# Kernel tuning notes

Hardware: AMD Instinct MI355X
Metric: run time of the kernel (lower is better)

The kernel has to match this reference:

```python
import jax, jax.numpy as jnp
import numpy as np

B, T, D, H, C = 256, 512, 64, 512, 1

def setup_inputs() -> dict:
    key = jax.random.key(0)
    ks = jax.random.split(key, 12)
    return {
        "x": jax.random.normal(ks[0], (B, T, D), jnp.float32),
        "w_ih_mu": jax.random.normal(ks[1], (D, 4 * H), jnp.float32) * 0.1,
        "w_ih_rho": jax.random.normal(ks[2], (D, 4 * H), jnp.float32) - 6.0,
        "eps_ih": jax.random.normal(ks[3], (D, 4 * H), jnp.float32),
        "w_hh_mu": jax.random.normal(ks[4], (H, 4 * H), jnp.float32) * 0.1,
        "w_hh_rho": jax.random.normal(ks[5], (H, 4 * H), jnp.float32) - 6.0,
        "eps_hh": jax.random.normal(ks[6], (H, 4 * H), jnp.float32),
        "b_mu": jax.random.normal(ks[7], (4 * H,), jnp.float32) * 0.1,
        "b_rho": jax.random.normal(ks[8], (4 * H,), jnp.float32) - 6.0,
        "eps_b": jax.random.normal(ks[9], (4 * H,), jnp.float32),
        "lin_w": jax.random.normal(ks[10], (C, H), jnp.float32) * 0.04,
        "lin_b": jax.random.normal(ks[11], (C,), jnp.float32) * 0.04,
    }

def _sample(mu, rho, eps):
    # blitz reparameterization: sigma = log1p(exp(rho))
    return mu + jnp.log1p(jnp.exp(rho)) * eps

def reference(x, w_ih_mu, w_ih_rho, eps_ih, w_hh_mu, w_hh_rho, eps_hh,
              b_mu, b_rho, eps_b, lin_w, lin_b):
    w_ih = _sample(w_ih_mu, w_ih_rho, eps_ih)
    w_hh = _sample(w_hh_mu, w_hh_rho, eps_hh)
    b = _sample(b_mu, b_rho, eps_b)

    # precompute input projections for all timesteps: [T, B, 4H]
    x_proj = jnp.einsum('btd,dg->tbg', x, w_ih) + b

    def step(carry, xp_t):
        h, c = carry
        gates = xp_t + h @ w_hh                      # [B, 4H]
        i, f, g, o = jnp.split(gates, 4, axis=-1)
        i = jax.nn.sigmoid(i)
        f = jax.nn.sigmoid(f)
        g = jnp.tanh(g)
        o = jax.nn.sigmoid(o)
        c = f * c + i * g
        h = o * jnp.tanh(c)
        return (h, c), None

    h0 = jnp.zeros((x.shape[0], w_hh.shape[0]), x.dtype)
    (h_last, _), _ = jax.lax.scan(step, (h0, h0), x_proj)
    # original takes outputs[:, -1, :] == last hidden state, then Linear
    return h_last @ lin_w.T + lin_b
```

## Files before the change

kernel.cpp:

```cpp
#include <hip/hip_runtime.h>

typedef unsigned short u16;
typedef unsigned long long u64;
typedef short v8s __attribute__((ext_vector_type(8)));
typedef float v4f __attribute__((ext_vector_type(4)));
typedef unsigned v2u __attribute__((ext_vector_type(2)));

#define Bb 256
#define Tt 512
#define Dd 64
#define Hh 512
#define G4 2048

#define NGROUP 16
#define NCHUNK 16
#define BT 16
#define HC 32
#define NCOL 128

#define WHH_S 520
#define WIH_S 72
#define SMEM_BYTES (NCOL*WHH_S*2 + NCOL*WIH_S*2)

#define MFMA(a,b,c) __builtin_amdgcn_mfma_f32_16x16x32_bf16((a),(b),(c),0,0,0)

__device__ __forceinline__ u16 f2bf(float f) {
  unsigned u = __float_as_uint(f);
  unsigned r = (u + 0x7fffu + ((u >> 16) & 1u)) >> 16;
  return (u16)r;
}
__device__ __forceinline__ float bf2f(u16 v) {
  return __uint_as_float(((unsigned)v) << 16);
}
__device__ __forceinline__ float sigm(float x) { return 1.0f / (1.0f + __expf(-x)); }
__device__ __forceinline__ float tanh_f(float x) {
  float a = fabsf(x);
  float e = __expf(-2.0f * a);
  float r = (1.0f - e) / (1.0f + e);
  return copysignf(r, x);
}
__device__ __forceinline__ float softplus_f(float x) { return log1pf(__expf(x)); }

__global__ void k_prep(const float* __restrict__ x, u16* __restrict__ x_bf,
                       unsigned* __restrict__ flags)
{
  if (blockIdx.x < 2) {
    int i = blockIdx.x * 256 + threadIdx.x;
    if (i < NGROUP * NCHUNK * 2) flags[i] = 0u;
  }
  const int N4 = Tt * Bb * Dd / 4;
  int stride = gridDim.x * blockDim.x;
  for (int i = blockIdx.x * blockDim.x + threadIdx.x; i < N4; i += stride) {
    int idx = i * 4;
    int t = idx >> 14;
    int rem = idx & 16383;
    int b = rem >> 6;
    int d = rem & 63;
    float4 v = *(const float4*)(x + (size_t)b * (Tt * Dd) + t * Dd + d);
    unsigned lo = (unsigned)f2bf(v.x) | ((unsigned)f2bf(v.y) << 16);
    unsigned hi = (unsigned)f2bf(v.z) | ((unsigned)f2bf(v.w) << 16);
    *(uint2*)(x_bf + idx) = make_uint2(lo, hi);
  }
}

__global__ __launch_bounds__(128, 1) void lstm_main(
    const float* __restrict__ whh_mu, const float* __restrict__ whh_rho, const float* __restrict__ whh_eps,
    const float* __restrict__ wih_mu, const float* __restrict__ wih_rho, const float* __restrict__ wih_eps,
    const float* __restrict__ b_mu,  const float* __restrict__ b_rho,  const float* __restrict__ b_eps,
    const u16* __restrict__ x_bf, u16* __restrict__ h_buf, unsigned* __restrict__ flags)
{
  extern __shared__ char smem[];
  u16* w_hh_lds = (u16*)smem;
  u16* w_ih_lds = w_hh_lds + NCOL * WHH_S;

  const int tid   = threadIdx.x;
  const int g     = blockIdx.x & 15;
  const int chunk = blockIdx.x >> 4;
  const int b0    = g * BT;
  const int j0    = chunk * HC;

  {
    const int lc = tid;
    const int gcol = (lc >> 5) * Hh + j0 + (lc & 31);
    #pragma unroll 4
    for (int k = 0; k < Hh; ++k) {
      int gi = k * G4 + gcol;
      float w = whh_mu[gi] + softplus_f(whh_rho[gi]) * whh_eps[gi];
      w_hh_lds[lc * WHH_S + k] = f2bf(w);
    }
    #pragma unroll 4
    for (int k = 0; k < Dd; ++k) {
      int gi = k * G4 + gcol;
      float w = wih_mu[gi] + softplus_f(wih_rho[gi]) * wih_eps[gi];
      w_ih_lds[lc * WIH_S + k] = f2bf(w);
    }
  }

  const int lane = tid & 63;
  const int wv   = tid >> 6;
  const int ln   = lane & 15;
  const int q    = lane >> 4;
  const int ko   = q * 8;

  const u16* WhP[4]; const u16* WxP[4];
  #pragma unroll
  for (int gt = 0; gt < 4; ++gt) {
    int rt = gt * 2 + wv;
    WhP[gt] = w_hh_lds + (rt * 16 + ln) * WHH_S + ko;
    WxP[gt] = w_ih_lds + (rt * 16 + ln) * WIH_S + ko;
  }

  const int bat = b0 + ln;

  float bs[4][4];
  #pragma unroll
  for (int gt = 0; gt < 4; ++gt)
    #pragma unroll
    for (int r = 0; r < 4; ++r) {
      int colg = gt * Hh + j0 + wv * 16 + q * 4 + r;
      bs[gt][r] = b_mu[colg] + softplus_f(b_rho[colg]) * b_eps[colg];
    }

  float cc[4] = {0.f, 0.f, 0.f, 0.f};
  unsigned* const fgrp2 = flags + g * (NCHUNK * 2);
  const unsigned* fp2 = fgrp2 + (lane & 31);
  __syncthreads();

  for (int t = 0; t < Tt; ++t) {
    v4f ac0 = {0.f,0.f,0.f,0.f}, ac1 = {0.f,0.f,0.f,0.f};
    v4f ac2 = {0.f,0.f,0.f,0.f}, ac3 = {0.f,0.f,0.f,0.f};

    {
      const u16* xb = x_bf + (size_t)t * (Bb * Dd) + bat * Dd + ko;
      #pragma unroll
      for (int ks = 0; ks < 2; ++ks) {
        v8s xf = *(const v8s*)(xb + ks * 32);
        ac0 = MFMA(*(const v8s*)(WxP[0] + ks * 32), xf, ac0);
        ac1 = MFMA(*(const v8s*)(WxP[1] + ks * 32), xf, ac1);
        ac2 = MFMA(*(const v8s*)(WxP[2] + ks * 32), xf, ac2);
        ac3 = MFMA(*(const v8s*)(WxP[3] + ks * 32), xf, ac3);
      }
    }

    if (t > 0) {
      const u16* hb = h_buf + (t & 1) * (Bb * Hh) + bat * Hh + ko;
      unsigned done = 0, todo = 0;
      v8s buf[16];
      for (;;) {
        unsigned pv = 0;
        bool needPoll = (done | todo) != 0xFFFFu;
        if (needPoll) {
          asm volatile("global_load_dword %0, %1, off sc0 sc1"
                       : "=v"(pv) : "v"(fp2));
        }
        #pragma unroll
        for (int c = 0; c < 16; ++c)
          if (todo & (1u << c)) {
            asm volatile("global_load_dwordx4 %0, %1, off offset:%c2 sc0 sc1"
                         : "=v"(buf[c]) : "v"(hb), "i"(c * 64));
          }
        asm volatile("s_waitcnt vmcnt(0)");
        if (needPoll) {
          asm volatile("" : "+v"(pv));
        }
        #pragma unroll
        for (int c = 0; c < 16; ++c)
          if (todo & (1u << c)) {
            asm volatile("" : "+v"(buf[c]));
            ac0 = MFMA(*(const v8s*)(WhP[0] + c * 32), buf[c], ac0);
            ac1 = MFMA(*(const v8s*)(WhP[1] + c * 32), buf[c], ac1);
            ac2 = MFMA(*(const v8s*)(WhP[2] + c * 32), buf[c], ac2);
            ac3 = MFMA(*(const v8s*)(WhP[3] + c * 32), buf[c], ac3);
          }
        done |= todo;
        if (done == 0xFFFFu) break;
        u64 bal = __ballot((int)(pv >= (unsigned)t));
        unsigned lo = (unsigned)bal;
        unsigned ready = lo & (lo >> 16) & 0xFFFFu;
        todo = ready & ~done;
      }
    }

    {
      u16 hv[4];
      #pragma unroll
      for (int r = 0; r < 4; ++r) {
        float ig = sigm  (ac0[r] + bs[0][r]);
        float fg = sigm  (ac1[r] + bs[1][r]);
        float gg = tanh_f(ac2[r] + bs[2][r]);
        float og = sigm  (ac3[r] + bs[3][r]);
        cc[r] = fg * cc[r] + ig * gg;
        hv[r] = f2bf(og * tanh_f(cc[r]));
      }
      v2u qv;
      qv[0] = (unsigned)hv[0] | ((unsigned)hv[1] << 16);
      qv[1] = (unsigned)hv[2] | ((unsigned)hv[3] << 16);
      u16* hp = h_buf + ((t + 1) & 1) * (Bb * Hh) + bat * Hh
              + j0 + wv * 16 + q * 4;
      asm volatile("global_store_dwordx2 %0, %1, off sc0 sc1"
                   :: "v"(hp), "v"(qv) : "memory");
    }

    asm volatile("s_waitcnt vmcnt(0)" ::: "memory");
    if (lane == 0) {
      unsigned tv = (unsigned)(t + 1);
      unsigned* fq = &fgrp2[wv * 16 + chunk];
      asm volatile("global_store_dword %0, %1, off sc0 sc1"
                   :: "v"(fq), "v"(tv) : "memory");
    }
  }
}

__global__ void k_out(const u16* __restrict__ h, const float* __restrict__ lw,
                      const float* __restrict__ lb, float* __restrict__ out)
{
  int b = blockIdx.x * 64 + threadIdx.x;
  if (b >= Bb) return;
  const u16* hr = h + b * Hh;
  float acc = 0.f;
  #pragma unroll 8
  for (int k = 0; k < Hh; ++k) acc += bf2f(hr[k]) * lw[k];
  out[b] = acc + lb[0];
}

extern "C" void kernel_launch(void* const* d_in, const int* in_sizes, int n_in,
                              void* d_out, int out_size, void* d_ws, size_t ws_size,
                              hipStream_t stream)
{
  (void)in_sizes; (void)n_in; (void)out_size; (void)ws_size;
  const float* x       = (const float*)d_in[0];
  const float* wih_mu  = (const float*)d_in[1];
  const float* wih_rho = (const float*)d_in[2];
  const float* wih_eps = (const float*)d_in[3];
  const float* whh_mu  = (const float*)d_in[4];
  const float* whh_rho = (const float*)d_in[5];
  const float* whh_eps = (const float*)d_in[6];
  const float* b_mu    = (const float*)d_in[7];
  const float* b_rho   = (const float*)d_in[8];
  const float* b_eps   = (const float*)d_in[9];
  const float* lin_w   = (const float*)d_in[10];
  const float* lin_b   = (const float*)d_in[11];
  float* out = (float*)d_out;

  u16* x_bf  = (u16*)d_ws;
  u16* h_buf = x_bf + (size_t)Tt * Bb * Dd;
  unsigned* flags = (unsigned*)(h_buf + 2 * Bb * Hh);

  k_prep<<<2048, 256, 0, stream>>>(x, x_bf, flags);

  hipFuncSetAttribute(reinterpret_cast<const void*>(lstm_main),
                      hipFuncAttributeMaxDynamicSharedMemorySize, SMEM_BYTES);
  lstm_main<<<NGROUP * NCHUNK, 128, SMEM_BYTES, stream>>>(
      whh_mu, whh_rho, whh_eps, wih_mu, wih_rho, wih_eps,
      b_mu, b_rho, b_eps, x_bf, h_buf, flags);

  k_out<<<(Bb + 63) / 64, 64, 0, stream>>>(h_buf, lin_w, lin_b, out);
}
```

Measured before the change: 2.473 ms.

## Split K dimension across waves with LDS reduction in recurrent LSTM step

Each wave now computes all 8 gate row tiles over half of the K dimension (256 of the hidden inputs and 32 of the input features) instead of 4 row tiles over the full K. The partial sums are exchanged through an LDS buffer with two block barriers per timestep. Each wave then waits on flags only for its own half of the h chunks, which shortens the dependency chain and lets the two waves consume producer data independently. In exchange each step adds LDS traffic, two __syncthreads calls, and twice as many accumulator registers.

```diff
diff --git a/kernel.cpp b/kernel.cpp
--- a/kernel.cpp
+++ b/kernel.cpp
@@ -20,7 +20,7 @@
 
 #define WHH_S 520
 #define WIH_S 72
-#define SMEM_BYTES (NCOL*WHH_S*2 + NCOL*WIH_S*2)
+#define SMEM_BYTES (NCOL*WHH_S*2 + NCOL*WIH_S*2 + 8192)
 
 #define MFMA(a,b,c) __builtin_amdgcn_mfma_f32_16x16x32_bf16((a),(b),(c),0,0,0)
 
@@ -70,8 +70,9 @@
     const u16* __restrict__ x_bf, u16* __restrict__ h_buf, unsigned* __restrict__ flags)
 {
   extern __shared__ char smem[];
-  u16* w_hh_lds = (u16*)smem;
-  u16* w_ih_lds = w_hh_lds + NCOL * WHH_S;
+  u16*   w_hh_lds = (u16*)smem;
+  u16*   w_ih_lds = w_hh_lds + NCOL * WHH_S;
+  float* pb       = (float*)(w_ih_lds + NCOL * WIH_S);
 
   const int tid   = threadIdx.x;
   const int g     = blockIdx.x & 15;
@@ -102,12 +103,11 @@
   const int q    = lane >> 4;
   const int ko   = q * 8;
 
-  const u16* WhP[4]; const u16* WxP[4];
+  const u16* WhB[8]; const u16* WxB[8];
   #pragma unroll
-  for (int gt = 0; gt < 4; ++gt) {
-    int rt = gt * 2 + wv;
-    WhP[gt] = w_hh_lds + (rt * 16 + ln) * WHH_S + ko;
-    WxP[gt] = w_ih_lds + (rt * 16 + ln) * WIH_S + ko;
+  for (int rt = 0; rt < 8; ++rt) {
+    WhB[rt] = w_hh_lds + (rt * 16 + ln) * WHH_S + wv * 256 + ko;
+    WxB[rt] = w_ih_lds + (rt * 16 + ln) * WIH_S + wv * 32 + ko;
   }
 
   const int bat = b0 + ln;
@@ -123,38 +123,35 @@
 
   float cc[4] = {0.f, 0.f, 0.f, 0.f};
   unsigned* const fgrp2 = flags + g * (NCHUNK * 2);
-  const unsigned* fp2 = fgrp2 + (lane & 31);
+  const unsigned* fp2 = fgrp2 + ((lane >> 3) & 1) * 16 + wv * 8 + (lane & 7);
   __syncthreads();
 
   for (int t = 0; t < Tt; ++t) {
-    v4f ac0 = {0.f,0.f,0.f,0.f}, ac1 = {0.f,0.f,0.f,0.f};
-    v4f ac2 = {0.f,0.f,0.f,0.f}, ac3 = {0.f,0.f,0.f,0.f};
+    v4f acc[8];
+    #pragma unroll
+    for (int rt = 0; rt < 8; ++rt) acc[rt] = (v4f){0.f,0.f,0.f,0.f};
 
     {
-      const u16* xb = x_bf + (size_t)t * (Bb * Dd) + bat * Dd + ko;
-      #pragma unroll
-      for (int ks = 0; ks < 2; ++ks) {
-        v8s xf = *(const v8s*)(xb + ks * 32);
-        ac0 = MFMA(*(const v8s*)(WxP[0] + ks * 32), xf, ac0);
-        ac1 = MFMA(*(const v8s*)(WxP[1] + ks * 32), xf, ac1);
-        ac2 = MFMA(*(const v8s*)(WxP[2] + ks * 32), xf, ac2);
-        ac3 = MFMA(*(const v8s*)(WxP[3] + ks * 32), xf, ac3);
-      }
+      const u16* xb = x_bf + (size_t)t * (Bb * Dd) + bat * Dd + wv * 32 + ko;
+      v8s xf = *(const v8s*)xb;
+      #pragma unroll
+      for (int rt = 0; rt < 8; ++rt)
+        acc[rt] = MFMA(*(const v8s*)WxB[rt], xf, acc[rt]);
     }
 
     if (t > 0) {
-      const u16* hb = h_buf + (t & 1) * (Bb * Hh) + bat * Hh + ko;
+      const u16* hb = h_buf + (t & 1) * (Bb * Hh) + bat * Hh + wv * 256 + ko;
       unsigned done = 0, todo = 0;
-      v8s buf[16];
+      v8s buf[8];
       for (;;) {
         unsigned pv = 0;
-        bool needPoll = (done | todo) != 0xFFFFu;
+        bool needPoll = (done | todo) != 0xFFu;
         if (needPoll) {
           asm volatile("global_load_dword %0, %1, off sc0 sc1"
                        : "=v"(pv) : "v"(fp2));
         }
         #pragma unroll
-        for (int c = 0; c < 16; ++c)
+        for (int c = 0; c < 8; ++c)
           if (todo & (1u << c)) {
             asm volatile("global_load_dwordx4 %0, %1, off offset:%c2 sc0 sc1"
                          : "=v"(buf[c]) : "v"(hb), "i"(c * 64));
@@ -164,31 +161,48 @@
           asm volatile("" : "+v"(pv));
         }
         #pragma unroll
-        for (int c = 0; c < 16; ++c)
+        for (int c = 0; c < 8; ++c)
           if (todo & (1u << c)) {
             asm volatile("" : "+v"(buf[c]));
-            ac0 = MFMA(*(const v8s*)(WhP[0] + c * 32), buf[c], ac0);
-            ac1 = MFMA(*(const v8s*)(WhP[1] + c * 32), buf[c], ac1);
-            ac2 = MFMA(*(const v8s*)(WhP[2] + c * 32), buf[c], ac2);
-            ac3 = MFMA(*(const v8s*)(WhP[3] + c * 32), buf[c], ac3);
+            #pragma unroll
+            for (int rt = 0; rt < 8; ++rt)
+              acc[rt] = MFMA(*(const v8s*)(WhB[rt] + c * 32), buf[c], acc[rt]);
           }
         done |= todo;
-        if (done == 0xFFFFu) break;
+        if (done == 0xFFu) break;
         u64 bal = __ballot((int)(pv >= (unsigned)t));
         unsigned lo = (unsigned)bal;
-        unsigned ready = lo & (lo >> 16) & 0xFFFFu;
+        unsigned ready = lo & (lo >> 8) & 0xFFu;
         todo = ready & ~done;
       }
     }
 
+    #pragma unroll
+    for (int gt = 0; gt < 4; ++gt) {
+      int pt = gt * 2 + (1 - wv);
+      #pragma unroll
+      for (int r = 0; r < 4; ++r)
+        pb[((wv * 4 + gt) * 4 + r) * 64 + lane] = acc[pt][r];
+    }
+    __syncthreads();
+    v4f ac[4];
+    #pragma unroll
+    for (int gt = 0; gt < 4; ++gt) {
+      int ot = gt * 2 + wv;
+      #pragma unroll
+      for (int r = 0; r < 4; ++r)
+        ac[gt][r] = acc[ot][r] + pb[(((1 - wv) * 4 + gt) * 4 + r) * 64 + lane];
+    }
+    __syncthreads();
+
     {
       u16 hv[4];
       #pragma unroll
       for (int r = 0; r < 4; ++r) {
-        float ig = sigm  (ac0[r] + bs[0][r]);
-        float fg = sigm  (ac1[r] + bs[1][r]);
-        float gg = tanh_f(ac2[r] + bs[2][r]);
-        float og = sigm  (ac3[r] + bs[3][r]);
+        float ig = sigm  (ac[0][r] + bs[0][r]);
+        float fg = sigm  (ac[1][r] + bs[1][r]);
+        float gg = tanh_f(ac[2][r] + bs[2][r]);
+        float og = sigm  (ac[3][r] + bs[3][r]);
         cc[r] = fg * cc[r] + ig * gg;
         hv[r] = f2bf(og * tanh_f(cc[r]));
       }
```

Measured after the change: 6.367 ms. 157% more time.
